# Kernel tuning notes

Measured on AMD Instinct MI355X. Metric: run time of the kernel, lower is better.

## Reference

```python
import jax, jax.numpy as jnp
import numpy as np

B, S, D = 8, 1024, 768
H, DK = 12, 64
DFF = 3072
EPS = 1e-5


def setup_inputs() -> dict:
    key = jax.random.key(0)
    ks = jax.random.split(key, 12)
    s = lambda fan_in: 1.0 / np.sqrt(fan_in)
    return {
        "x": jax.random.normal(ks[0], (B, S, D), jnp.float32),
        "Wq": jax.random.normal(ks[1], (D, D), jnp.float32) * s(D),
        "Wk": jax.random.normal(ks[2], (D, D), jnp.float32) * s(D),
        "Wv": jax.random.normal(ks[3], (D, D), jnp.float32) * s(D),
        "Wo": jax.random.normal(ks[4], (D, D), jnp.float32) * s(D),
        "g1": jnp.ones((D,), jnp.float32),
        "b1": jnp.zeros((D,), jnp.float32),
        "g2": jnp.ones((D,), jnp.float32),
        "b2": jnp.zeros((D,), jnp.float32),
        "W1": jax.random.normal(ks[5], (D, DFF), jnp.float32) * s(D),
        "bW1": jnp.zeros((DFF,), jnp.float32),
        "W2": jax.random.normal(ks[6], (DFF, D), jnp.float32) * s(DFF),
        "bW2": jnp.zeros((D,), jnp.float32),
    }


def _layernorm(x, g, b):
    mu = x.mean(-1, keepdims=True)
    var = ((x - mu) ** 2).mean(-1, keepdims=True)
    return (x - mu) * jax.lax.rsqrt(var + EPS) * g + b


def reference(x, Wq, Wk, Wv, Wo, g1, b1, g2, b2, W1, bW1, W2, bW2):
    scale = DK ** (-0.5)
    # pre-norm attention block
    h = _layernorm(x, g1, b1)
    q = (h @ Wq).reshape(B, S, H, DK)
    k = (h @ Wk).reshape(B, S, H, DK)
    v = (h @ Wv).reshape(B, S, H, DK)
    logits = jnp.einsum("bqhd,bkhd->bhqk", q, k) * scale  # [B,H,S,S]
    weights = jax.nn.softmax(logits, axis=-1)
    attn = jnp.einsum("bhqk,bkhd->bqhd", weights, v).reshape(B, S, D)
    x = x + attn @ Wo
    # pre-norm FFN block
    h = _layernorm(x, g2, b2)
    h = jax.nn.gelu(h @ W1 + bW1, approximate=False)
    x = x + h @ W2 + bW2
    return x
```

## Files before the change

### kernel.cpp

```cpp
#include <hip/hip_runtime.h>
#include <cstdint>
#include <cstddef>

#define B_   8
#define S_   1024
#define D_   768
#define H_   12
#define DK_  64
#define DFF_ 3072
#define M_   (B_*S_)

typedef __attribute__((ext_vector_type(8))) short  short8;
typedef __attribute__((ext_vector_type(4))) short  short4v;
typedef __attribute__((ext_vector_type(8))) __bf16 bf16x8;
typedef __attribute__((ext_vector_type(4))) float  f32x4;
typedef __attribute__((ext_vector_type(4))) unsigned uint4v;
typedef __attribute__((ext_vector_type(2))) unsigned uint2v;

__device__ __forceinline__ unsigned short f2bf(float f) {
    unsigned u = __builtin_bit_cast(unsigned, f);
    u += 0x7FFFu + ((u >> 16) & 1u);
    return (unsigned short)(u >> 16);
}

__device__ __forceinline__ unsigned pkbf(float a, float b) {
    unsigned short ua = __builtin_bit_cast(unsigned short, (__bf16)a);
    unsigned short ub = __builtin_bit_cast(unsigned short, (__bf16)b);
    return (unsigned)ua | ((unsigned)ub << 16);
}

__device__ __forceinline__ f32x4 mfma16(short8 a, short8 b, f32x4 c) {
    return __builtin_amdgcn_mfma_f32_16x16x32_bf16(
        __builtin_bit_cast(bf16x8, a), __builtin_bit_cast(bf16x8, b), c, 0, 0, 0);
}

__device__ __forceinline__ void gload16(const void* g, void* l) {
    auto gp = reinterpret_cast<const __attribute__((address_space(1))) unsigned*>(
        reinterpret_cast<uintptr_t>(g));
    auto lp = reinterpret_cast<__attribute__((address_space(3))) unsigned*>(
        reinterpret_cast<uintptr_t>(l));
    __builtin_amdgcn_global_load_lds(gp, lp, 16, 0, 0);
}

__device__ __forceinline__ float gelu_f(float v) {
    return 0.5f * v * (1.0f + erff(v * 0.70710678118654752f));
}

__global__ __launch_bounds__(256) void wtrans4_kernel(
    const float* __restrict__ W0, const float* __restrict__ W1,
    const float* __restrict__ W2, const float* __restrict__ W3,
    unsigned short* __restrict__ Wt)
{
    __shared__ float tile[32][33];
    int z = blockIdx.z;
    const float* W = (z == 0) ? W0 : (z == 1) ? W1 : (z == 2) ? W2 : W3;
    unsigned short* dst = Wt + (size_t)z * 768 * 768;
    int n0 = blockIdx.x * 32, k0 = blockIdx.y * 32;
    int tx = threadIdx.x, ty = threadIdx.y;
#pragma unroll
    for (int j = 0; j < 4; ++j)
        tile[ty + j*8][tx] = W[(size_t)(k0 + ty + j*8) * 768 + n0 + tx];
    __syncthreads();
#pragma unroll
    for (int j = 0; j < 4; ++j)
        dst[(size_t)(n0 + ty + j*8) * 768 + k0 + tx] = f2bf(tile[tx][ty + j*8]);
}

__global__ __launch_bounds__(256) void wtrans_kernel(
    const float* __restrict__ W, unsigned short* __restrict__ Wt, int K, int N)
{
    __shared__ float tile[32][33];
    int n0 = blockIdx.x * 32, k0 = blockIdx.y * 32;
    int tx = threadIdx.x, ty = threadIdx.y;
#pragma unroll
    for (int j = 0; j < 4; ++j)
        tile[ty + j*8][tx] = W[(size_t)(k0 + ty + j*8) * N + n0 + tx];
    __syncthreads();
#pragma unroll
    for (int j = 0; j < 4; ++j)
        Wt[(size_t)(n0 + ty + j*8) * K + k0 + tx] = f2bf(tile[tx][ty + j*8]);
}

__global__ __launch_bounds__(256) void ln_kernel(
    const float* __restrict__ x, const float* __restrict__ g,
    const float* __restrict__ b, unsigned short* __restrict__ out)
{
    int row = blockIdx.x, t = threadIdx.x;
    const float* xr = x + (size_t)row * D_;
    float v[3];
#pragma unroll
    for (int i = 0; i < 3; ++i) v[i] = xr[t + i*256];
    float s  = v[0] + v[1] + v[2];
    float ss = v[0]*v[0] + v[1]*v[1] + v[2]*v[2];
#pragma unroll
    for (int d = 1; d < 64; d <<= 1) { s += __shfl_xor(s, d); ss += __shfl_xor(ss, d); }
    __shared__ float red[8];
    int w = t >> 6, lane = t & 63;
    if (lane == 0) { red[w] = s; red[4 + w] = ss; }
    __syncthreads();
    s  = red[0] + red[1] + red[2] + red[3];
    ss = red[4] + red[5] + red[6] + red[7];
    float mu   = s * (1.0f / D_);
    float var  = ss * (1.0f / D_) - mu * mu;
    float rstd = rsqrtf(var + 1e-5f);
    unsigned short* orow = out + (size_t)row * D_;
#pragma unroll
    for (int i = 0; i < 3; ++i) {
        int c = t + i*256;
        orow[c] = f2bf((v[i] - mu) * rstd * g[c] + b[c]);
    }
}

template<int BN, int EPI>
__global__ __launch_bounds__(256, 2) void gemm_kernel(
    const unsigned short* __restrict__ A, const unsigned short* __restrict__ Wt,
    const float* __restrict__ bias, const float* __restrict__ resid,
    void* __restrict__ outp, int N, int K)
{
    __shared__ unsigned short Al[2][128*64];
    __shared__ unsigned short Bl[2][BN*64];
    constexpr int NJ = BN / 64;
    const int nbn = N / BN;
    const int nwg = gridDim.x;
    const int p = blockIdx.x;
    const int bid = (p & 7) * (nwg >> 3) + (p >> 3);
    const int bm = bid / nbn, bn = bid % nbn;
    const int t = threadIdx.x;
    const int lane = t & 63, w = t >> 6;
    const int wm = w >> 1, wn = w & 1;
    const int lr = lane & 15, lh = lane >> 4;
    const char* aBase = (const char*)(A  + (size_t)(bm*128) * K);
    const char* bBase = (const char*)(Wt + (size_t)(bn*BN)  * K);

    f32x4 acc[4][2*NJ] = {};

    auto stage = [&](int kt, int buf) {
        const int k0b = kt << 7;
#pragma unroll
        for (int shot = 0; shot < 4; ++shot) {
            int d = shot*4096 + t*16;
            int row = d >> 7;
            int ch  = ((d >> 4) & 7) ^ (row & 7);
            gload16(aBase + (size_t)row*(K*2) + k0b + ch*16, (char*)&Al[buf][0] + d);
        }
#pragma unroll
        for (int shot = 0; shot < 2*NJ; ++shot) {
            int d = shot*4096 + t*16;
            int row = d >> 7;
            int ch  = ((d >> 4) & 7) ^ (row & 7);
            gload16(bBase + (size_t)row*(K*2) + k0b + ch*16, (char*)&Bl[buf][0] + d);
        }
    };

    const int nk = K >> 6;
    stage(0, 0);
    stage(1, 1);

    for (int it = 0; it < nk; ++it) {
        const int buf = it & 1;
        if (it + 1 < nk) {
            if constexpr (BN == 128) asm volatile("s_waitcnt vmcnt(8)" ::: "memory");
            else                     asm volatile("s_waitcnt vmcnt(6)" ::: "memory");
        } else {
            asm volatile("s_waitcnt vmcnt(0)" ::: "memory");
        }
        __builtin_amdgcn_s_barrier();

        short8 af[2][4], bf[2][2*NJ];
#pragma unroll
        for (int kk = 0; kk < 2; ++kk) {
#pragma unroll
            for (int i = 0; i < 4; ++i)
                af[kk][i] = *reinterpret_cast<const short8*>(
                    &Al[buf][(wm*64 + i*16 + lr)*64 + (((kk*4 + lh) ^ (lr & 7))*8)]);
#pragma unroll
            for (int j = 0; j < 2*NJ; ++j)
                bf[kk][j] = *reinterpret_cast<const short8*>(
                    &Bl[buf][(wn*(32*NJ) + j*16 + lr)*64 + (((kk*4 + lh) ^ (lr & 7))*8)]);
        }
        __builtin_amdgcn_s_setprio(1);
#pragma unroll
        for (int kk = 0; kk < 2; ++kk)
#pragma unroll
            for (int i = 0; i < 4; ++i)
#pragma unroll
                for (int j = 0; j < 2*NJ; ++j)
                    acc[i][j] = mfma16(af[kk][i], bf[kk][j], acc[i][j]);
        __builtin_amdgcn_s_setprio(0);
        __builtin_amdgcn_s_barrier();
        if (it + 2 < nk) stage(it + 2, buf);
    }

#pragma unroll
    for (int i = 0; i < 4; ++i) {
#pragma unroll
        for (int r = 0; r < 4; ++r) {
            int row = bm*128 + wm*64 + i*16 + lh*4 + r;
#pragma unroll
            for (int j = 0; j < 2*NJ; ++j) {
                int col = bn*BN + wn*(32*NJ) + j*16 + lr;
                float v = acc[i][j][r];
                if (EPI == 0) {
                    ((unsigned short*)outp)[(size_t)row*N + col] = f2bf(v);
                } else if (EPI == 1) {
                    v += bias[col];
                    v = gelu_f(v);
                    ((unsigned short*)outp)[(size_t)row*N + col] = f2bf(v);
                } else {
                    if (bias) v += bias[col];
                    v += resid[(size_t)row*N + col];
                    ((float*)outp)[(size_t)row*N + col] = v;
                }
            }
        }
    }
}

__global__ __launch_bounds__(256) void vtrans_kernel(
    const unsigned short* __restrict__ qkv, unsigned short* __restrict__ vt)
{
    __shared__ unsigned short tl[64][65];
    int bid = blockIdx.x;
    int sblk = bid & 15, bh = bid >> 4;
    int b = bh / H_, h = bh % H_;
    int t = threadIdx.x, tx = t & 63, ty = t >> 6;
    int s0 = sblk * 64;
#pragma unroll
    for (int j = 0; j < 16; ++j) {
        int s = j*4 + ty;
        tl[s][tx] = qkv[(size_t)(b*S_ + s0 + s)*2304 + 1536 + h*64 + tx];
    }
    __syncthreads();
#pragma unroll
    for (int j = 0; j < 16; ++j) {
        int dk = j*4 + ty;
        vt[((size_t)bh*64 + dk)*S_ + s0 + tx] = tl[tx][dk];
    }
}

__global__ __launch_bounds__(256, 3) void attn_kernel(
    const unsigned short* __restrict__ qkv, const unsigned short* __restrict__ vt,
    unsigned short* __restrict__ out)
{
    __shared__ unsigned short Kl[2][64*64];
    __shared__ unsigned short Vl[2][64*64];

    const int p = blockIdx.x;
    const int l = (p & 7) * 96 + (p >> 3);
    const int qb = l & 7, bh = l >> 3;
    const int b = bh / H_, h = bh % H_;
    const int t = threadIdx.x, lane = t & 63, w = t >> 6;
    const int lr = lane & 15, lh = lane >> 4;
    const int sz = (lr & 7) << 3;

    const float SC = 0.125f * 1.44269504089f;

    const int qrow0 = qb*128 + w*32;
    short8 bq[2][2];
#pragma unroll
    for (int qi = 0; qi < 2; ++qi) {
        const unsigned short* qp = qkv + (size_t)(b*S_ + qrow0 + qi*16 + lr)*2304 + h*64;
#pragma unroll
        for (int c = 0; c < 2; ++c)
            bq[qi][c] = *reinterpret_cast<const short8*>(&qp[c*32 + lh*8]);
    }

    float m_run[2] = {-1e30f, -1e30f};
    float l_run[2] = {0.f, 0.f};
    f32x4 o[2][4] = {};

    const char* kgbase = (const char*)qkv;
    const char* vgbase = (const char*)vt;

    auto stage = [&](int kb, int buf) {
        const int ks = kb * 64;
#pragma unroll
        for (int shot = 0; shot < 2; ++shot) {
            int d = shot*4096 + t*16;
            int row = d >> 7;
            int colb = d & 127;
            int sc = colb ^ ((row & 7) << 4);
            const char* ksrc = kgbase + ((size_t)(b*S_ + ks + row)*2304 + 768 + h*64)*2 + sc;
            gload16(ksrc, (char*)&Kl[buf][0] + d);
            const char* vsrc = vgbase + ((size_t)(bh*64 + row)*1024 + ks)*2 + sc;
            gload16(vsrc, (char*)&Vl[buf][0] + d);
        }
    };

    stage(0, 0);
    asm volatile("s_waitcnt vmcnt(0)" ::: "memory");
    __builtin_amdgcn_s_barrier();

    for (int kb = 0; kb < 16; ++kb) {
        const int buf = kb & 1;
        if (kb < 15) stage(kb + 1, buf ^ 1);

        short8 ak[4][2];
#pragma unroll
        for (int j = 0; j < 4; ++j)
#pragma unroll
            for (int c = 0; c < 2; ++c)
                ak[j][c] = *reinterpret_cast<const short8*>(
                    &Kl[buf][(j*16 + lr)*64 + ((c*32 + lh*8) ^ sz)]);

        short8 av[4][2];
#pragma unroll
        for (int j = 0; j < 4; ++j) {
            const unsigned short* vrow = &Vl[buf][(j*16 + lr)*64];
#pragma unroll
            for (int ks = 0; ks < 2; ++ks) {
                short4v lo = *reinterpret_cast<const short4v*>(&vrow[(ks*32 + lh*4)      ^ sz]);
                short4v hi = *reinterpret_cast<const short4v*>(&vrow[(ks*32 + 16 + lh*4) ^ sz]);
                av[j][ks] = __builtin_shufflevector(lo, hi, 0,1,2,3,4,5,6,7);
            }
        }

#pragma unroll
        for (int qi = 0; qi < 2; ++qi) {
            f32x4 s[4];
            __builtin_amdgcn_s_setprio(1);
#pragma unroll
            for (int j = 0; j < 4; ++j) {
                f32x4 z = {0.f, 0.f, 0.f, 0.f};
                z = mfma16(ak[j][0], bq[qi][0], z);
                z = mfma16(ak[j][1], bq[qi][1], z);
                s[j] = z;
            }
            __builtin_amdgcn_s_setprio(0);

            float m01 = fmaxf(fmaxf(s[0][0], s[0][1]), fmaxf(s[0][2], s[0][3]));
            float m1  = fmaxf(fmaxf(s[1][0], s[1][1]), fmaxf(s[1][2], s[1][3]));
            float m2  = fmaxf(fmaxf(s[2][0], s[2][1]), fmaxf(s[2][2], s[2][3]));
            float m3  = fmaxf(fmaxf(s[3][0], s[3][1]), fmaxf(s[3][2], s[3][3]));
            float mt = fmaxf(fmaxf(m01, m1), fmaxf(m2, m3)) * SC;
            mt = fmaxf(mt, __shfl_xor(mt, 16));
            mt = fmaxf(mt, __shfl_xor(mt, 32));

            if (__any(mt > m_run[qi] + 8.0f)) {
                float mn = fmaxf(m_run[qi], mt);
                float a  = exp2f(m_run[qi] - mn);
                m_run[qi] = mn;
                l_run[qi] *= a;
#pragma unroll
                for (int j = 0; j < 4; ++j)
#pragma unroll
                    for (int r = 0; r < 4; ++r) o[qi][j][r] *= a;
            }

            const float negm = -m_run[qi];
            float rs = 0.f;
#pragma unroll
            for (int j = 0; j < 4; ++j)
#pragma unroll
                for (int r = 0; r < 4; ++r) {
                    float pv = exp2f(__builtin_fmaf(s[j][r], SC, negm));
                    s[j][r] = pv;
                    rs += pv;
                }
            l_run[qi] += rs;

            uint4v u0 = { pkbf(s[0][0], s[0][1]), pkbf(s[0][2], s[0][3]),
                          pkbf(s[1][0], s[1][1]), pkbf(s[1][2], s[1][3]) };
            uint4v u1 = { pkbf(s[2][0], s[2][1]), pkbf(s[2][2], s[2][3]),
                          pkbf(s[3][0], s[3][1]), pkbf(s[3][2], s[3][3]) };
            short8 pb0 = __builtin_bit_cast(short8, u0);
            short8 pb1 = __builtin_bit_cast(short8, u1);

            __builtin_amdgcn_s_setprio(1);
#pragma unroll
            for (int j = 0; j < 4; ++j) {
                o[qi][j] = mfma16(av[j][0], pb0, o[qi][j]);
                o[qi][j] = mfma16(av[j][1], pb1, o[qi][j]);
            }
            __builtin_amdgcn_s_setprio(0);
        }

        asm volatile("s_waitcnt vmcnt(0)" ::: "memory");
        __builtin_amdgcn_s_barrier();
    }

#pragma unroll
    for (int qi = 0; qi < 2; ++qi) {
        float ls = l_run[qi];
        ls += __shfl_xor(ls, 16);
        ls += __shfl_xor(ls, 32);
        float inv = 1.0f / ls;
        int q = qrow0 + qi*16 + lr;
        unsigned short* orow = out + (size_t)(b*S_ + q)*D_ + h*64;
#pragma unroll
        for (int j = 0; j < 4; ++j) {
            uint2v vv = { pkbf(o[qi][j][0]*inv, o[qi][j][1]*inv),
                          pkbf(o[qi][j][2]*inv, o[qi][j][3]*inv) };
            *reinterpret_cast<uint2v*>(&orow[j*16 + lh*4]) = vv;
        }
    }
}

extern "C" void kernel_launch(void* const* d_in, const int* in_sizes, int n_in,
                              void* d_out, int out_size, void* d_ws, size_t ws_size,
                              hipStream_t stream)
{
    (void)in_sizes; (void)n_in; (void)out_size; (void)ws_size;
    const float* x   = (const float*)d_in[0];
    const float* Wq  = (const float*)d_in[1];
    const float* Wk  = (const float*)d_in[2];
    const float* Wv  = (const float*)d_in[3];
    const float* Wo  = (const float*)d_in[4];
    const float* g1  = (const float*)d_in[5];
    const float* b1  = (const float*)d_in[6];
    const float* g2  = (const float*)d_in[7];
    const float* b2  = (const float*)d_in[8];
    const float* W1  = (const float*)d_in[9];
    const float* bW1 = (const float*)d_in[10];
    const float* W2  = (const float*)d_in[11];
    const float* bW2 = (const float*)d_in[12];
    float* out = (float*)d_out;

    char* ws = (char*)d_ws;
    unsigned short* wt_qkv = (unsigned short*)(ws);
    unsigned short* wt_o   = (unsigned short*)(ws + 3538944);
    unsigned short* wt_1   = (unsigned short*)(ws + 4718592);
    unsigned short* wt_2   = (unsigned short*)(ws + 9437184);
    unsigned short* slotA  = (unsigned short*)(ws + 14155776);
    unsigned short* qkv    = (unsigned short*)(ws + 26738688);
    unsigned short* vt     = (unsigned short*)(ws + 64487424);
    unsigned short* ffm    = qkv;

    dim3 tb(32, 8);
    wtrans4_kernel<<<dim3(24,24,4), tb, 0, stream>>>(Wq, Wk, Wv, Wo, wt_qkv);
    wtrans_kernel<<<dim3(96,24), tb, 0, stream>>>(W1, wt_1, 768, 3072);
    wtrans_kernel<<<dim3(24,96), tb, 0, stream>>>(W2, wt_2, 3072, 768);

    ln_kernel<<<M_, 256, 0, stream>>>(x, g1, b1, slotA);
    gemm_kernel<128,0><<<64*18, 256, 0, stream>>>(slotA, wt_qkv, nullptr, nullptr, qkv, 2304, 768);
    vtrans_kernel<<<1536, 256, 0, stream>>>(qkv, vt);
    attn_kernel<<<768, 256, 0, stream>>>(qkv, vt, slotA);
    gemm_kernel<64,2><<<64*12, 256, 0, stream>>>(slotA, wt_o, nullptr, x, (void*)out, 768, 768);
    ln_kernel<<<M_, 256, 0, stream>>>(out, g2, b2, slotA);
    gemm_kernel<128,1><<<64*24, 256, 0, stream>>>(slotA, wt_1, bW1, nullptr, ffm, 3072, 768);
    gemm_kernel<64,2><<<64*12, 256, 0, stream>>>(ffm, wt_2, bW2, out, (void*)out, 768, 3072);
}
```

Before: 305.9 us.

## Use 256x128 tile, 512-thread GEMM for FFN up-projection and precompute load addresses

Adds a 512-thread GEMM variant with a 256x128 output tile (8 waves, each 64x64) and uses it for the W1+GELU projection, so each B tile is reused across twice as many rows. Both GEMM kernels now compute their swizzled global load addresses once before the K loop instead of on every stage, which cuts per-iteration integer work. The larger tile raises LDS use to 96KB per block and register pressure, which may limit occupancy. The other launch counts are only rewritten as literals and are unchanged.

```diff
diff --git a/kernel.cpp b/kernel.cpp
--- a/kernel.cpp
+++ b/kernel.cpp
@@ -120,6 +120,7 @@
     __shared__ unsigned short Al[2][128*64];
     __shared__ unsigned short Bl[2][BN*64];
     constexpr int NJ = BN / 64;
+    constexpr int ASH = 4, BSH = 2*NJ;
     const int nbn = N / BN;
     const int nwg = gridDim.x;
     const int p = blockIdx.x;
@@ -132,24 +133,32 @@
     const char* aBase = (const char*)(A  + (size_t)(bm*128) * K);
     const char* bBase = (const char*)(Wt + (size_t)(bn*BN)  * K);
 
+    uintptr_t aAdr[ASH], bAdr[BSH];
+#pragma unroll
+    for (int s = 0; s < ASH; ++s) {
+        int d = s*4096 + t*16;
+        int row = d >> 7;
+        int ch  = ((d >> 4) & 7) ^ (row & 7);
+        aAdr[s] = (uintptr_t)aBase + (size_t)row*(K*2) + ch*16;
+    }
+#pragma unroll
+    for (int s = 0; s < BSH; ++s) {
+        int d = s*4096 + t*16;
+        int row = d >> 7;
+        int ch  = ((d >> 4) & 7) ^ (row & 7);
+        bAdr[s] = (uintptr_t)bBase + (size_t)row*(K*2) + ch*16;
+    }
+
     f32x4 acc[4][2*NJ] = {};
 
     auto stage = [&](int kt, int buf) {
         const int k0b = kt << 7;
 #pragma unroll
-        for (int shot = 0; shot < 4; ++shot) {
-            int d = shot*4096 + t*16;
-            int row = d >> 7;
-            int ch  = ((d >> 4) & 7) ^ (row & 7);
-            gload16(aBase + (size_t)row*(K*2) + k0b + ch*16, (char*)&Al[buf][0] + d);
-        }
-#pragma unroll
-        for (int shot = 0; shot < 2*NJ; ++shot) {
-            int d = shot*4096 + t*16;
-            int row = d >> 7;
-            int ch  = ((d >> 4) & 7) ^ (row & 7);
-            gload16(bBase + (size_t)row*(K*2) + k0b + ch*16, (char*)&Bl[buf][0] + d);
-        }
+        for (int s = 0; s < ASH; ++s)
+            gload16((const void*)(aAdr[s] + k0b), (char*)&Al[buf][0] + s*4096 + t*16);
+#pragma unroll
+        for (int s = 0; s < BSH; ++s)
+            gload16((const void*)(bAdr[s] + k0b), (char*)&Bl[buf][0] + s*4096 + t*16);
     };
 
     const int nk = K >> 6;
@@ -216,6 +225,114 @@
     }
 }
 
+template<int EPI>
+__global__ __launch_bounds__(512, 2) void gemmb_kernel(
+    const unsigned short* __restrict__ A, const unsigned short* __restrict__ Wt,
+    const float* __restrict__ bias, const float* __restrict__ resid,
+    void* __restrict__ outp, int N, int K)
+{
+    __shared__ unsigned short Al[2][256*64];
+    __shared__ unsigned short Bl[2][128*64];
+    const int nbn = N >> 7;
+    const int nwg = gridDim.x;
+    const int p = blockIdx.x;
+    const int bid = (p & 7) * (nwg >> 3) + (p >> 3);
+    const int bm = bid / nbn, bn = bid % nbn;
+    const int t = threadIdx.x;
+    const int lane = t & 63, w = t >> 6;
+    const int wm = w >> 1, wn = w & 1;
+    const int lr = lane & 15, lh = lane >> 4;
+    const char* aBase = (const char*)(A  + (size_t)(bm*256) * K);
+    const char* bBase = (const char*)(Wt + (size_t)(bn*128) * K);
+
+    uintptr_t aAdr[4], bAdr[2];
+#pragma unroll
+    for (int s = 0; s < 4; ++s) {
+        int d = s*8192 + t*16;
+        int row = d >> 7;
+        int ch  = ((d >> 4) & 7) ^ (row & 7);
+        aAdr[s] = (uintptr_t)aBase + (size_t)row*(K*2) + ch*16;
+    }
+#pragma unroll
+    for (int s = 0; s < 2; ++s) {
+        int d = s*8192 + t*16;
+        int row = d >> 7;
+        int ch  = ((d >> 4) & 7) ^ (row & 7);
+        bAdr[s] = (uintptr_t)bBase + (size_t)row*(K*2) + ch*16;
+    }
+
+    f32x4 acc[4][4] = {};
+
+    auto stage = [&](int kt, int buf) {
+        const int k0b = kt << 7;
+#pragma unroll
+        for (int s = 0; s < 4; ++s)
+            gload16((const void*)(aAdr[s] + k0b), (char*)&Al[buf][0] + s*8192 + t*16);
+#pragma unroll
+        for (int s = 0; s < 2; ++s)
+            gload16((const void*)(bAdr[s] + k0b), (char*)&Bl[buf][0] + s*8192 + t*16);
+    };
+
+    const int nk = K >> 6;
+    stage(0, 0);
+    stage(1, 1);
+
+    for (int it = 0; it < nk; ++it) {
+        const int buf = it & 1;
+        if (it + 1 < nk) asm volatile("s_waitcnt vmcnt(6)" ::: "memory");
+        else             asm volatile("s_waitcnt vmcnt(0)" ::: "memory");
+        __builtin_amdgcn_s_barrier();
+
+        short8 af[2][4], bf[2][4];
+#pragma unroll
+        for (int kk = 0; kk < 2; ++kk) {
+#pragma unroll
+            for (int i = 0; i < 4; ++i)
+                af[kk][i] = *reinterpret_cast<const short8*>(
+                    &Al[buf][(wm*64 + i*16 + lr)*64 + (((kk*4 + lh) ^ (lr & 7))*8)]);
+#pragma unroll
+            for (int j = 0; j < 4; ++j)
+                bf[kk][j] = *reinterpret_cast<const short8*>(
+                    &Bl[buf][(wn*64 + j*16 + lr)*64 + (((kk*4 + lh) ^ (lr & 7))*8)]);
+        }
+        __builtin_amdgcn_s_setprio(1);
+#pragma unroll
+        for (int kk = 0; kk < 2; ++kk)
+#pragma unroll
+            for (int i = 0; i < 4; ++i)
+#pragma unroll
+                for (int j = 0; j < 4; ++j)
+                    acc[i][j] = mfma16(af[kk][i], bf[kk][j], acc[i][j]);
+        __builtin_amdgcn_s_setprio(0);
+        __builtin_amdgcn_s_barrier();
+        if (it + 2 < nk) stage(it + 2, buf);
+    }
+
+#pragma unroll
+    for (int i = 0; i < 4; ++i) {
+#pragma unroll
+        for (int r = 0; r < 4; ++r) {
+            int row = bm*256 + wm*64 + i*16 + lh*4 + r;
+#pragma unroll
+            for (int j = 0; j < 4; ++j) {
+                int col = bn*128 + wn*64 + j*16 + lr;
+                float v = acc[i][j][r];
+                if (EPI == 0) {
+                    ((unsigned short*)outp)[(size_t)row*N + col] = f2bf(v);
+                } else if (EPI == 1) {
+                    v += bias[col];
+                    v = gelu_f(v);
+                    ((unsigned short*)outp)[(size_t)row*N + col] = f2bf(v);
+                } else {
+                    if (bias) v += bias[col];
+                    v += resid[(size_t)row*N + col];
+                    ((float*)outp)[(size_t)row*N + col] = v;
+                }
+            }
+        }
+    }
+}
+
 __global__ __launch_bounds__(256) void vtrans_kernel(
     const unsigned short* __restrict__ qkv, unsigned short* __restrict__ vt)
 {
@@ -432,11 +549,11 @@
     wtrans_kernel<<<dim3(24,96), tb, 0, stream>>>(W2, wt_2, 3072, 768);
 
     ln_kernel<<<M_, 256, 0, stream>>>(x, g1, b1, slotA);
-    gemm_kernel<128,0><<<64*18, 256, 0, stream>>>(slotA, wt_qkv, nullptr, nullptr, qkv, 2304, 768);
+    gemm_kernel<128,0><<<1152, 256, 0, stream>>>(slotA, wt_qkv, nullptr, nullptr, qkv, 2304, 768);
     vtrans_kernel<<<1536, 256, 0, stream>>>(qkv, vt);
     attn_kernel<<<768, 256, 0, stream>>>(qkv, vt, slotA);
-    gemm_kernel<64,2><<<64*12, 256, 0, stream>>>(slotA, wt_o, nullptr, x, (void*)out, 768, 768);
+    gemm_kernel<64,2><<<768, 256, 0, stream>>>(slotA, wt_o, nullptr, x, (void*)out, 768, 768);
     ln_kernel<<<M_, 256, 0, stream>>>(out, g2, b2, slotA);
-    gemm_kernel<128,1><<<64*24, 256, 0, stream>>>(slotA, wt_1, bW1, nullptr, ffm, 3072, 768);
-    gemm_kernel<64,2><<<64*12, 256, 0, stream>>>(ffm, wt_2, bW2, out, (void*)out, 768, 3072);
-}
+    gemmb_kernel<1><<<768, 512, 0, stream>>>(slotA, wt_1, bW1, nullptr, ffm, 3072, 768);
+    gemm_kernel<64,2><<<768, 256, 0, stream>>>(ffm, wt_2, bW2, out, (void*)out, 768, 3072);
+}
```

After: 310.3 us. Within noise of the previous version (+1.4%).
